# Performance work log

Measured on AMD Instinct MI355X. Metric: run time of the kernel, lower is better.

The kernel has to match this reference:

```python
import jax, jax.numpy as jnp
import numpy as np

B, I, O, T, L, K, PAD = 16, 256, 256, 512, 8192, 7, 3
EPS = 1e-8


def setup_inputs() -> dict:
    key = jax.random.key(0)
    ks = jax.random.split(key, 7)
    bx = jax.random.normal(ks[0], (B, I, L), dtype=jnp.float32)
    t = jax.random.normal(ks[1], (B, T), dtype=jnp.float32)
    # depthwise conv weight: torch Conv1d(groups=I) weight is (I, 1, K)
    conv_w = jax.random.normal(ks[2], (I, 1, K), dtype=jnp.float32) * (1.0 / np.sqrt(K))
    # 1x1 proj: torch Conv1d weight (O, I, 1) -> store as (O, I)
    proj_w = jax.random.normal(ks[3], (O, I), dtype=jnp.float32) * (1.0 / np.sqrt(I))
    proj_b = jax.random.normal(ks[4], (O,), dtype=jnp.float32) * 0.01
    # Linear(t_dim -> in_dim)
    mod_w = jax.random.normal(ks[5], (I, T), dtype=jnp.float32) * (1.0 / np.sqrt(T))
    mod_b = jax.random.normal(ks[6], (I,), dtype=jnp.float32) * 0.01
    return {"bx": bx, "t": t, "conv_w": conv_w, "proj_w": proj_w,
            "proj_b": proj_b, "mod_w": mod_w, "mod_b": mod_b}


def reference(bx, t, conv_w, proj_w, proj_b, mod_w, mod_b):
    # modulation: (B, I)
    mod = t @ mod_w.T + mod_b
    # per-sample modulated 1x1 weights: (B, O, I)
    bw = proj_w[None, :, :] * (mod[:, None, :] + 1.0)
    # demodulation (L2 over input dim, kernel dim is size 1)
    demod = jax.lax.rsqrt(jnp.sum(bw * bw, axis=2) + EPS)  # (B, O)
    bw = bw * demod[:, :, None]
    # depthwise conv over length, 'same' padding (kernel 7, pad 3)
    xc = jax.lax.conv_general_dilated(
        bx, conv_w,
        window_strides=(1,), padding=[(PAD, PAD)],
        dimension_numbers=('NCH', 'OIH', 'NCH'),
        feature_group_count=I)  # (B, I, L)
    # per-sample grouped 1x1 conv == batched matmul
    out = jnp.einsum('boi,bil->bol', bw, xc) + proj_b[None, :, None]
    return out
```

## Files before the change

kernel.cpp:

```cpp
#include <hip/hip_runtime.h>
#include <hip/hip_bf16.h>

#define B_ 16
#define I_ 256
#define O_ 256
#define T_ 512
#define L_ 8192
#define K_ 7
#define PAD_ 3
#define BN 64
#define LDK 264

typedef unsigned short u16;
typedef unsigned int u32;
typedef __attribute__((ext_vector_type(8))) short short8;
typedef __attribute__((ext_vector_type(4))) float f32x4;

__device__ inline u16 f2bf(float f) {
    union { float f; u32 u; } v; v.f = f;
    u32 r = v.u + 0x7FFF + ((v.u >> 16) & 1);
    return (u16)(r >> 16);
}

__global__ void mod_kernel(const float* __restrict__ t, const float* __restrict__ mod_w,
                           const float* __restrict__ mod_b, float* __restrict__ mod) {
    int g = blockIdx.x, b = blockIdx.y;
    int lane = threadIdx.x & 63, wv = threadIdx.x >> 6;
    const float* tb = t + b * T_;
    #pragma unroll
    for (int q = 0; q < 4; ++q) {
        int i = g * 16 + wv * 4 + q;
        const float* wr = mod_w + (size_t)i * T_;
        float s = 0.f;
        #pragma unroll
        for (int u = 0; u < 8; ++u) s += wr[lane + u * 64] * tb[lane + u * 64];
        #pragma unroll
        for (int d = 32; d; d >>= 1) s += __shfl_down(s, d);
        if (lane == 0) mod[b * I_ + i] = s + mod_b[i];
    }
}

__global__ void wmod_kernel(const float* __restrict__ proj_w, const float* __restrict__ mod,
                            u16* __restrict__ Wb) {
    int og = blockIdx.x, b = blockIdx.y;
    int lane = threadIdx.x & 63, wv = threadIdx.x >> 6;
    const float* mrow = mod + b * I_;
    #pragma unroll
    for (int q = 0; q < 4; ++q) {
        int o = og * 16 + wv * 4 + q;
        const float* pw = proj_w + (size_t)o * I_;
        float4 pv = *(const float4*)(pw + lane * 4);
        float4 mv = *(const float4*)(mrow + lane * 4);
        float v0 = pv.x * (mv.x + 1.f);
        float v1 = pv.y * (mv.y + 1.f);
        float v2 = pv.z * (mv.z + 1.f);
        float v3 = pv.w * (mv.w + 1.f);
        float ss = v0*v0 + v1*v1 + v2*v2 + v3*v3;
        #pragma unroll
        for (int d = 32; d; d >>= 1) ss += __shfl_xor(ss, d);
        float dem = rsqrtf(ss + 1e-8f);
        u32 lo = (u32)f2bf(v0 * dem) | ((u32)f2bf(v1 * dem) << 16);
        u32 hi = (u32)f2bf(v2 * dem) | ((u32)f2bf(v3 * dem) << 16);
        *(uint2*)(Wb + (size_t)(b * O_ + o) * I_ + lane * 4) = make_uint2(lo, hi);
    }
}

__global__ __launch_bounds__(256) void main_kernel(
    const float* __restrict__ bx, const float* __restrict__ conv_w,
    const u16* __restrict__ Wb, const float* __restrict__ proj_b,
    float* __restrict__ out)
{
    __shared__ __align__(16) u16 Xs[BN * LDK];

    const int tile = blockIdx.x;
    const int b = blockIdx.y;
    const int l0 = tile * BN;
    const int tid = threadIdx.x;
    const int lane = tid & 63;
    const int wv = tid >> 6;
    const int mlane = lane & 15;
    const int quad = lane >> 4;

    const int rq = tid >> 2;
    const int lq = tid & 3;
    const int i0 = rq * 4;
    const float* bxr = bx + (size_t)b * I_ * L_;
    const bool interior = (l0 >= 4) && (l0 + 72 <= L_);

    float wr[4][K_];
    #pragma unroll
    for (int di = 0; di < 4; ++di)
        #pragma unroll
        for (int j = 0; j < K_; ++j)
            wr[di][j] = conv_w[(i0 + di) * K_ + j];

    for (int it = 0; it < 4; ++it) {
        const int lb = it * 16 + lq * 4;
        u16 hv[4][4];
        #pragma unroll
        for (int di = 0; di < 4; ++di) {
            const float* row = bxr + (size_t)(i0 + di) * L_ + l0;
            float x[12];
            if (interior) {
                const float4* rp = (const float4*)(row + lb - 4);
                float4 w0 = rp[0], w1 = rp[1], w2 = rp[2];
                x[0]=w0.x; x[1]=w0.y; x[2]=w0.z; x[3]=w0.w;
                x[4]=w1.x; x[5]=w1.y; x[6]=w1.z; x[7]=w1.w;
                x[8]=w2.x; x[9]=w2.y; x[10]=w2.z; x[11]=w2.w;
            } else {
                #pragma unroll
                for (int w = 0; w < 12; ++w) {
                    int p = l0 + lb - 4 + w;
                    x[w] = (p >= 0 && p < L_) ? row[lb - 4 + w] : 0.f;
                }
            }
            #pragma unroll
            for (int dl = 0; dl < 4; ++dl) {
                float a = 0.f;
                #pragma unroll
                for (int j = 0; j < K_; ++j) a += wr[di][j] * x[dl + 1 + j];
                hv[dl][di] = f2bf(a);
            }
        }
        #pragma unroll
        for (int dl = 0; dl < 4; ++dl) {
            int n = lb + dl;
            u32 lo = (u32)hv[dl][0] | ((u32)hv[dl][1] << 16);
            u32 hi = (u32)hv[dl][2] | ((u32)hv[dl][3] << 16);
            *(uint2*)(&Xs[n * LDK + i0]) = make_uint2(lo, hi);
        }
    }
    __syncthreads();

    f32x4 acc[4][4];
    #pragma unroll
    for (int r = 0; r < 4; ++r)
        #pragma unroll
        for (int c = 0; c < 4; ++c)
            acc[r][c] = (f32x4){0.f, 0.f, 0.f, 0.f};

    const u16* Wrow = Wb + (size_t)(b * O_ + wv * 64 + mlane) * I_;

    for (int kb = 0; kb < 8; ++kb) {
        const int koff = kb * 32 + quad * 8;
        short8 a[4], bbf[4];
        #pragma unroll
        for (int r = 0; r < 4; ++r)
            a[r] = *(const short8*)(Wrow + r * 16 * I_ + koff);
        #pragma unroll
        for (int c = 0; c < 4; ++c)
            bbf[c] = *(const short8*)(&Xs[(c * 16 + mlane) * LDK + koff]);
        #pragma unroll
        for (int r = 0; r < 4; ++r)
            #pragma unroll
            for (int c = 0; c < 4; ++c)
                acc[r][c] = __builtin_amdgcn_mfma_f32_16x16x32_bf16(a[r], bbf[c], acc[r][c], 0, 0, 0);
    }

    float* outb = out + (size_t)b * O_ * L_;
    #pragma unroll
    for (int r = 0; r < 4; ++r) {
        const int obase = wv * 64 + r * 16 + quad * 4;
        #pragma unroll
        for (int p = 0; p < 4; ++p) {
            const int o = obase + p;
            const float bias = proj_b[o];
            float* orow = outb + (size_t)o * L_ + l0 + mlane;
            #pragma unroll
            for (int c = 0; c < 4; ++c)
                orow[c * 16] = acc[r][c][p] + bias;
        }
    }
}

extern "C" void kernel_launch(void* const* d_in, const int* in_sizes, int n_in,
                              void* d_out, int out_size, void* d_ws, size_t ws_size,
                              hipStream_t stream) {
    const float* bx     = (const float*)d_in[0];
    const float* t      = (const float*)d_in[1];
    const float* conv_w = (const float*)d_in[2];
    const float* proj_w = (const float*)d_in[3];
    const float* proj_b = (const float*)d_in[4];
    const float* mod_w  = (const float*)d_in[5];
    const float* mod_b  = (const float*)d_in[6];
    float* out = (float*)d_out;

    float* mod = (float*)d_ws;
    u16*   Wb  = (u16*)((char*)d_ws + 16384);

    mod_kernel<<<dim3(16, 16), 256, 0, stream>>>(t, mod_w, mod_b, mod);
    wmod_kernel<<<dim3(16, 16), 256, 0, stream>>>(proj_w, mod, Wb);
    main_kernel<<<dim3(128, 16), 256, 0, stream>>>(bx, conv_w, Wb, proj_b, out);
}
```

Measured before the change: 316.4 us.

## Split fused conv+GEMM kernel into separate conv and GEMM kernels via workspace

Splits the fused depthwise-conv plus MFMA GEMM kernel into two kernels when the workspace is large enough. The conv kernel writes a bf16 transposed tile to global memory, and the GEMM kernel reads it back directly without LDS. The aim is to decouple the conv phase's register and LDS pressure from the GEMM phase so that occupancy and latency hiding improve in each. In exchange it adds about 64 MB of extra global write and read traffic plus one more launch. The fused kernel remains as a fallback.

```diff
diff --git a/kernel.cpp b/kernel.cpp
--- a/kernel.cpp
+++ b/kernel.cpp
@@ -9,6 +9,7 @@
 #define K_ 7
 #define PAD_ 3
 #define BN 64
+#define NTILE 128
 #define LDK 264
 
 typedef unsigned short u16;
@@ -65,10 +66,8 @@
     }
 }
 
-__global__ __launch_bounds__(256) void main_kernel(
-    const float* __restrict__ bx, const float* __restrict__ conv_w,
-    const u16* __restrict__ Wb, const float* __restrict__ proj_b,
-    float* __restrict__ out)
+__global__ __launch_bounds__(256) void conv_kernel(
+    const float* __restrict__ bx, const float* __restrict__ conv_w, u16* __restrict__ xt)
 {
     __shared__ __align__(16) u16 Xs[BN * LDK];
 
@@ -76,10 +75,6 @@
     const int b = blockIdx.y;
     const int l0 = tile * BN;
     const int tid = threadIdx.x;
-    const int lane = tid & 63;
-    const int wv = tid >> 6;
-    const int mlane = lane & 15;
-    const int quad = lane >> 4;
 
     const int rq = tid >> 2;
     const int lq = tid & 3;
@@ -94,6 +89,7 @@
         for (int j = 0; j < K_; ++j)
             wr[di][j] = conv_w[(i0 + di) * K_ + j];
 
+    #pragma unroll
     for (int it = 0; it < 4; ++it) {
         const int lb = it * 16 + lq * 4;
         u16 hv[4][4];
@@ -132,6 +128,138 @@
     }
     __syncthreads();
 
+    u16* dst = xt + (size_t)(b * NTILE + tile) * (BN * I_);
+    #pragma unroll
+    for (int r = 0; r < 8; ++r) {
+        int g = tid + r * 256;
+        int n = g >> 5;
+        int c = g & 31;
+        uint4 v = *(const uint4*)(&Xs[n * LDK + c * 8]);
+        *(uint4*)(dst + (size_t)g * 8) = v;
+    }
+}
+
+__global__ __launch_bounds__(256) void gemm_kernel(
+    const u16* __restrict__ xt, const u16* __restrict__ Wb,
+    const float* __restrict__ proj_b, float* __restrict__ out)
+{
+    const int tile = blockIdx.x;
+    const int b = blockIdx.y;
+    const int l0 = tile * BN;
+    const int lane = threadIdx.x & 63;
+    const int wv = threadIdx.x >> 6;
+    const int mlane = lane & 15;
+    const int quad = lane >> 4;
+
+    f32x4 acc[4][4];
+    #pragma unroll
+    for (int r = 0; r < 4; ++r)
+        #pragma unroll
+        for (int c = 0; c < 4; ++c)
+            acc[r][c] = (f32x4){0.f, 0.f, 0.f, 0.f};
+
+    const u16* Wrow  = Wb + (size_t)(b * O_ + wv * 64 + mlane) * I_;
+    const u16* Xtile = xt + (size_t)(b * NTILE + tile) * (BN * I_);
+
+    for (int kb = 0; kb < 8; ++kb) {
+        const int koff = kb * 32 + quad * 8;
+        short8 a[4], bbf[4];
+        #pragma unroll
+        for (int r = 0; r < 4; ++r)
+            a[r] = *(const short8*)(Wrow + r * 16 * I_ + koff);
+        #pragma unroll
+        for (int c = 0; c < 4; ++c)
+            bbf[c] = *(const short8*)(Xtile + (c * 16 + mlane) * I_ + koff);
+        #pragma unroll
+        for (int r = 0; r < 4; ++r)
+            #pragma unroll
+            for (int c = 0; c < 4; ++c)
+                acc[r][c] = __builtin_amdgcn_mfma_f32_16x16x32_bf16(a[r], bbf[c], acc[r][c], 0, 0, 0);
+    }
+
+    float* outb = out + (size_t)b * O_ * L_;
+    #pragma unroll
+    for (int r = 0; r < 4; ++r) {
+        const int obase = wv * 64 + r * 16 + quad * 4;
+        #pragma unroll
+        for (int p = 0; p < 4; ++p) {
+            const int o = obase + p;
+            const float bias = proj_b[o];
+            float* orow = outb + (size_t)o * L_ + l0 + mlane;
+            #pragma unroll
+            for (int c = 0; c < 4; ++c)
+                orow[c * 16] = acc[r][c][p] + bias;
+        }
+    }
+}
+
+__global__ __launch_bounds__(256) void main_kernel(
+    const float* __restrict__ bx, const float* __restrict__ conv_w,
+    const u16* __restrict__ Wb, const float* __restrict__ proj_b,
+    float* __restrict__ out)
+{
+    __shared__ __align__(16) u16 Xs[BN * LDK];
+
+    const int tile = blockIdx.x;
+    const int b = blockIdx.y;
+    const int l0 = tile * BN;
+    const int tid = threadIdx.x;
+    const int lane = tid & 63;
+    const int wv = tid >> 6;
+    const int mlane = lane & 15;
+    const int quad = lane >> 4;
+
+    const int rq = tid >> 2;
+    const int lq = tid & 3;
+    const int i0 = rq * 4;
+    const float* bxr = bx + (size_t)b * I_ * L_;
+    const bool interior = (l0 >= 4) && (l0 + 72 <= L_);
+
+    float wr[4][K_];
+    #pragma unroll
+    for (int di = 0; di < 4; ++di)
+        #pragma unroll
+        for (int j = 0; j < K_; ++j)
+            wr[di][j] = conv_w[(i0 + di) * K_ + j];
+
+    for (int it = 0; it < 4; ++it) {
+        const int lb = it * 16 + lq * 4;
+        u16 hv[4][4];
+        #pragma unroll
+        for (int di = 0; di < 4; ++di) {
+            const float* row = bxr + (size_t)(i0 + di) * L_ + l0;
+            float x[12];
+            if (interior) {
+                const float4* rp = (const float4*)(row + lb - 4);
+                float4 w0 = rp[0], w1 = rp[1], w2 = rp[2];
+                x[0]=w0.x; x[1]=w0.y; x[2]=w0.z; x[3]=w0.w;
+                x[4]=w1.x; x[5]=w1.y; x[6]=w1.z; x[7]=w1.w;
+                x[8]=w2.x; x[9]=w2.y; x[10]=w2.z; x[11]=w2.w;
+            } else {
+                #pragma unroll
+                for (int w = 0; w < 12; ++w) {
+                    int p = l0 + lb - 4 + w;
+                    x[w] = (p >= 0 && p < L_) ? row[lb - 4 + w] : 0.f;
+                }
+            }
+            #pragma unroll
+            for (int dl = 0; dl < 4; ++dl) {
+                float a = 0.f;
+                #pragma unroll
+                for (int j = 0; j < K_; ++j) a += wr[di][j] * x[dl + 1 + j];
+                hv[dl][di] = f2bf(a);
+            }
+        }
+        #pragma unroll
+        for (int dl = 0; dl < 4; ++dl) {
+            int n = lb + dl;
+            u32 lo = (u32)hv[dl][0] | ((u32)hv[dl][1] << 16);
+            u32 hi = (u32)hv[dl][2] | ((u32)hv[dl][3] << 16);
+            *(uint2*)(&Xs[n * LDK + i0]) = make_uint2(lo, hi);
+        }
+    }
+    __syncthreads();
+
     f32x4 acc[4][4];
     #pragma unroll
     for (int r = 0; r < 4; ++r)
@@ -185,10 +313,20 @@
     const float* mod_b  = (const float*)d_in[6];
     float* out = (float*)d_out;
 
+    const size_t OFF_WB = 16384;
+    const size_t OFF_XT = OFF_WB + (size_t)B_ * O_ * I_ * 2ull;
+    const size_t need   = OFF_XT + (size_t)B_ * NTILE * BN * I_ * 2ull;
+
     float* mod = (float*)d_ws;
-    u16*   Wb  = (u16*)((char*)d_ws + 16384);
+    u16*   Wb  = (u16*)((char*)d_ws + OFF_WB);
+    u16*   xt  = (u16*)((char*)d_ws + OFF_XT);
 
     mod_kernel<<<dim3(16, 16), 256, 0, stream>>>(t, mod_w, mod_b, mod);
     wmod_kernel<<<dim3(16, 16), 256, 0, stream>>>(proj_w, mod, Wb);
-    main_kernel<<<dim3(128, 16), 256, 0, stream>>>(bx, conv_w, Wb, proj_b, out);
-}
+    if (ws_size >= need) {
+        conv_kernel<<<dim3(NTILE, 16), 256, 0, stream>>>(bx, conv_w, xt);
+        gemm_kernel<<<dim3(NTILE, 16), 256, 0, stream>>>(xt, Wb, proj_b, out);
+    } else {
+        main_kernel<<<dim3(NTILE, 16), 256, 0, stream>>>(bx, conv_w, Wb, proj_b, out);
+    }
+}
```

Measured after the change: 366.3 us. +15.8%, slower.

## Split conv and GEMM into separate kernels with MFMA-swizzled global layouts

Applied to the files above, without the earlier changes.

Merges the modulation and demodulation kernels into one per-batch kernel that writes weights pre-swizzled in MFMA fragment order. The depthwise conv moves to its own kernel, which writes bf16 activations to global workspace in the same fragment-native layout. A new GEMM kernel loads fragments directly with coalesced 16-byte loads, double-buffers the k-loop in registers, and stages output through LDS so stores are float4 and row-contiguous. This removes the strided output stores and the per-tile LDS transpose, but adds a global round trip of the bf16 activations (about 64MB written and read).

```diff
diff --git a/kernel.cpp b/kernel.cpp
--- a/kernel.cpp
+++ b/kernel.cpp
@@ -7,9 +7,8 @@
 #define T_ 512
 #define L_ 8192
 #define K_ 7
-#define PAD_ 3
-#define BN 64
-#define LDK 264
+#define CT 1024
+#define NT 128
 
 typedef unsigned short u16;
 typedef unsigned int u32;
@@ -22,115 +21,121 @@
     return (u16)(r >> 16);
 }
 
-__global__ void mod_kernel(const float* __restrict__ t, const float* __restrict__ mod_w,
-                           const float* __restrict__ mod_b, float* __restrict__ mod) {
-    int g = blockIdx.x, b = blockIdx.y;
-    int lane = threadIdx.x & 63, wv = threadIdx.x >> 6;
+
+__global__ __launch_bounds__(256) void wmod_kernel(
+    const float* __restrict__ t, const float* __restrict__ mod_w, const float* __restrict__ mod_b,
+    const float* __restrict__ proj_w, u16* __restrict__ Wsw)
+{
+    __shared__ __align__(16) float mod_s[I_];
+    const int b = blockIdx.x, tid = threadIdx.x;
+
     const float* tb = t + b * T_;
-    #pragma unroll
-    for (int q = 0; q < 4; ++q) {
-        int i = g * 16 + wv * 4 + q;
-        const float* wr = mod_w + (size_t)i * T_;
-        float s = 0.f;
-        #pragma unroll
-        for (int u = 0; u < 8; ++u) s += wr[lane + u * 64] * tb[lane + u * 64];
-        #pragma unroll
-        for (int d = 32; d; d >>= 1) s += __shfl_down(s, d);
-        if (lane == 0) mod[b * I_ + i] = s + mod_b[i];
-    }
-}
-
-__global__ void wmod_kernel(const float* __restrict__ proj_w, const float* __restrict__ mod,
-                            u16* __restrict__ Wb) {
-    int og = blockIdx.x, b = blockIdx.y;
-    int lane = threadIdx.x & 63, wv = threadIdx.x >> 6;
-    const float* mrow = mod + b * I_;
-    #pragma unroll
-    for (int q = 0; q < 4; ++q) {
-        int o = og * 16 + wv * 4 + q;
-        const float* pw = proj_w + (size_t)o * I_;
-        float4 pv = *(const float4*)(pw + lane * 4);
-        float4 mv = *(const float4*)(mrow + lane * 4);
-        float v0 = pv.x * (mv.x + 1.f);
-        float v1 = pv.y * (mv.y + 1.f);
-        float v2 = pv.z * (mv.z + 1.f);
-        float v3 = pv.w * (mv.w + 1.f);
-        float ss = v0*v0 + v1*v1 + v2*v2 + v3*v3;
-        #pragma unroll
-        for (int d = 32; d; d >>= 1) ss += __shfl_xor(ss, d);
-        float dem = rsqrtf(ss + 1e-8f);
-        u32 lo = (u32)f2bf(v0 * dem) | ((u32)f2bf(v1 * dem) << 16);
-        u32 hi = (u32)f2bf(v2 * dem) | ((u32)f2bf(v3 * dem) << 16);
-        *(uint2*)(Wb + (size_t)(b * O_ + o) * I_ + lane * 4) = make_uint2(lo, hi);
-    }
-}
-
-__global__ __launch_bounds__(256) void main_kernel(
-    const float* __restrict__ bx, const float* __restrict__ conv_w,
-    const u16* __restrict__ Wb, const float* __restrict__ proj_b,
-    float* __restrict__ out)
+    const float* wr = mod_w + (size_t)tid * T_;
+    float s = 0.f;
+    #pragma unroll 8
+    for (int k = 0; k < T_ / 4; ++k) {
+        float4 w4 = *(const float4*)(wr + 4 * k);
+        float4 t4 = *(const float4*)(tb + 4 * k);
+        s += w4.x * t4.x + w4.y * t4.y + w4.z * t4.z + w4.w * t4.w;
+    }
+    mod_s[tid] = s + mod_b[tid];
+    __syncthreads();
+
+    const float* pw = proj_w + (size_t)tid * I_;
+    float ss = 0.f;
+    #pragma unroll 8
+    for (int k = 0; k < I_ / 4; ++k) {
+        float4 p = *(const float4*)(pw + 4 * k);
+        float4 m = *(const float4*)(&mod_s[4 * k]);
+        float a0 = p.x * (m.x + 1.f), a1 = p.y * (m.y + 1.f);
+        float a2 = p.z * (m.z + 1.f), a3 = p.w * (m.w + 1.f);
+        ss += a0 * a0 + a1 * a1 + a2 * a2 + a3 * a3;
+    }
+    const float dem = rsqrtf(ss + 1e-8f);
+    const int wv = tid >> 6, r = (tid >> 4) & 3, ml = tid & 15;
+    #pragma unroll 4
+    for (int oc = 0; oc < 32; ++oc) {
+        float4 p0 = *(const float4*)(pw + oc * 8);
+        float4 p1 = *(const float4*)(pw + oc * 8 + 4);
+        float4 m0 = *(const float4*)(&mod_s[oc * 8]);
+        float4 m1 = *(const float4*)(&mod_s[oc * 8 + 4]);
+        u32 q0 = (u32)f2bf(p0.x * (m0.x + 1.f) * dem) | ((u32)f2bf(p0.y * (m0.y + 1.f) * dem) << 16);
+        u32 q1 = (u32)f2bf(p0.z * (m0.z + 1.f) * dem) | ((u32)f2bf(p0.w * (m0.w + 1.f) * dem) << 16);
+        u32 q2 = (u32)f2bf(p1.x * (m1.x + 1.f) * dem) | ((u32)f2bf(p1.y * (m1.y + 1.f) * dem) << 16);
+        u32 q3 = (u32)f2bf(p1.z * (m1.z + 1.f) * dem) | ((u32)f2bf(p1.w * (m1.w + 1.f) * dem) << 16);
+        const int kb = oc >> 2, quad = oc & 3;
+        u16* dst = Wsw + ((((size_t)(b * 4 + wv) * 8 + kb) * 4 + r) * 64 + quad * 16 + ml) * 8;
+        *(uint4*)dst = make_uint4(q0, q1, q2, q3);
+    }
+}
+
+__global__ __launch_bounds__(256) void conv_kernel(
+    const float* __restrict__ bx, const float* __restrict__ conv_w, u16* __restrict__ Xsw)
 {
-    __shared__ __align__(16) u16 Xs[BN * LDK];
-
-    const int tile = blockIdx.x;
-    const int b = blockIdx.y;
-    const int l0 = tile * BN;
+    __shared__ __align__(16) u16 Os[CT * 8];
+    const int oct = blockIdx.x;
+    const int lg  = blockIdx.y;
+    const int b   = blockIdx.z;
     const int tid = threadIdx.x;
-    const int lane = tid & 63;
-    const int wv = tid >> 6;
-    const int mlane = lane & 15;
-    const int quad = lane >> 4;
-
-    const int rq = tid >> 2;
-    const int lq = tid & 3;
-    const int i0 = rq * 4;
-    const float* bxr = bx + (size_t)b * I_ * L_;
-    const bool interior = (l0 >= 4) && (l0 + 72 <= L_);
-
-    float wr[4][K_];
-    #pragma unroll
-    for (int di = 0; di < 4; ++di)
+    const int l0  = lg * CT;
+    const int lt  = l0 + tid * 4;
+    const float* base = bx + ((size_t)b * I_ + oct * 8) * L_;
+
+    float w[8][K_];
+    #pragma unroll
+    for (int ch = 0; ch < 8; ++ch)
         #pragma unroll
         for (int j = 0; j < K_; ++j)
-            wr[di][j] = conv_w[(i0 + di) * K_ + j];
-
-    for (int it = 0; it < 4; ++it) {
-        const int lb = it * 16 + lq * 4;
-        u16 hv[4][4];
-        #pragma unroll
-        for (int di = 0; di < 4; ++di) {
-            const float* row = bxr + (size_t)(i0 + di) * L_ + l0;
-            float x[12];
-            if (interior) {
-                const float4* rp = (const float4*)(row + lb - 4);
-                float4 w0 = rp[0], w1 = rp[1], w2 = rp[2];
-                x[0]=w0.x; x[1]=w0.y; x[2]=w0.z; x[3]=w0.w;
-                x[4]=w1.x; x[5]=w1.y; x[6]=w1.z; x[7]=w1.w;
-                x[8]=w2.x; x[9]=w2.y; x[10]=w2.z; x[11]=w2.w;
-            } else {
-                #pragma unroll
-                for (int w = 0; w < 12; ++w) {
-                    int p = l0 + lb - 4 + w;
-                    x[w] = (p >= 0 && p < L_) ? row[lb - 4 + w] : 0.f;
-                }
-            }
-            #pragma unroll
-            for (int dl = 0; dl < 4; ++dl) {
-                float a = 0.f;
-                #pragma unroll
-                for (int j = 0; j < K_; ++j) a += wr[di][j] * x[dl + 1 + j];
-                hv[dl][di] = f2bf(a);
-            }
+            w[ch][j] = conv_w[(oct * 8 + ch) * K_ + j];
+
+    const bool okL = (lt > 0);
+    const bool okR = (lt + 4 < L_);
+    u32 pk[4][4] = {};
+
+    #pragma unroll
+    for (int ch = 0; ch < 8; ++ch) {
+        const float* row = base + (size_t)ch * L_;
+        float4 za = okL ? *(const float4*)(row + lt - 4) : make_float4(0.f, 0.f, 0.f, 0.f);
+        float4 zb = *(const float4*)(row + lt);
+        float4 zc = okR ? *(const float4*)(row + lt + 4) : make_float4(0.f, 0.f, 0.f, 0.f);
+        float x[12] = {za.x, za.y, za.z, za.w, zb.x, zb.y, zb.z, zb.w, zc.x, zc.y, zc.z, zc.w};
+        #pragma unroll
+        for (int dl = 0; dl < 4; ++dl) {
+            float a = 0.f;
+            #pragma unroll
+            for (int j = 0; j < K_; ++j) a += w[ch][j] * x[dl + 1 + j];
+            pk[dl][ch >> 1] |= ((u32)f2bf(a)) << (16 * (ch & 1));
         }
-        #pragma unroll
-        for (int dl = 0; dl < 4; ++dl) {
-            int n = lb + dl;
-            u32 lo = (u32)hv[dl][0] | ((u32)hv[dl][1] << 16);
-            u32 hi = (u32)hv[dl][2] | ((u32)hv[dl][3] << 16);
-            *(uint2*)(&Xs[n * LDK + i0]) = make_uint2(lo, hi);
-        }
-    }
+    }
+    #pragma unroll
+    for (int dl = 0; dl < 4; ++dl)
+        *(uint4*)(&Os[(size_t)(tid * 4 + dl) * 8]) = make_uint4(pk[dl][0], pk[dl][1], pk[dl][2], pk[dl][3]);
     __syncthreads();
+
+    const int kb = oct >> 2, quad = oct & 3;
+    #pragma unroll
+    for (int pass = 0; pass < 4; ++pass) {
+        int idx = pass * 256 + tid;
+        int l = l0 + idx;
+        int tile = l >> 6, c = (l >> 4) & 3, ml = l & 15;
+        uint4 v = *(const uint4*)(&Os[(size_t)idx * 8]);
+        u16* dst = Xsw + ((((size_t)(b * NT + tile) * 8 + kb) * 4 + c) * 64 + quad * 16 + ml) * 8;
+        *(uint4*)dst = v;
+    }
+}
+
+__global__ __launch_bounds__(256) void gemm_kernel(
+    const u16* __restrict__ Xsw, const u16* __restrict__ Wsw,
+    const float* __restrict__ proj_b, float* __restrict__ out)
+{
+    __shared__ __align__(16) float Cs[64 * 68];
+    const int tile = blockIdx.x, b = blockIdx.y;
+    const int tid = threadIdx.x, lane = tid & 63, wv = tid >> 6;
+    const int ml = lane & 15, quad = lane >> 4;
+    const int l0 = tile * 64;
+
+    const u16* Ab = Wsw + ((size_t)(b * 4 + wv) * 8 * 4 * 64) * 8 + (size_t)lane * 8;
+    const u16* Bb = Xsw + ((size_t)(b * NT + tile) * 8 * 4 * 64) * 8 + (size_t)lane * 8;
 
     f32x4 acc[4][4];
     #pragma unroll
@@ -139,37 +144,47 @@
         for (int c = 0; c < 4; ++c)
             acc[r][c] = (f32x4){0.f, 0.f, 0.f, 0.f};
 
-    const u16* Wrow = Wb + (size_t)(b * O_ + wv * 64 + mlane) * I_;
-
+    short8 a[2][4], bb[2][4];
+    #pragma unroll
+    for (int r = 0; r < 4; ++r) a[0][r] = *(const short8*)(Ab + (size_t)r * 512);
+    #pragma unroll
+    for (int c = 0; c < 4; ++c) bb[0][c] = *(const short8*)(Bb + (size_t)c * 512);
+
+    #pragma unroll
     for (int kb = 0; kb < 8; ++kb) {
-        const int koff = kb * 32 + quad * 8;
-        short8 a[4], bbf[4];
+        const int cur = kb & 1, nxt = cur ^ 1;
+        if (kb < 7) {
+            #pragma unroll
+            for (int r = 0; r < 4; ++r) a[nxt][r] = *(const short8*)(Ab + (size_t)((kb + 1) * 4 + r) * 512);
+            #pragma unroll
+            for (int c = 0; c < 4; ++c) bb[nxt][c] = *(const short8*)(Bb + (size_t)((kb + 1) * 4 + c) * 512);
+        }
         #pragma unroll
         for (int r = 0; r < 4; ++r)
-            a[r] = *(const short8*)(Wrow + r * 16 * I_ + koff);
+            #pragma unroll
+            for (int c = 0; c < 4; ++c)
+                acc[r][c] = __builtin_amdgcn_mfma_f32_16x16x32_bf16(a[cur][r], bb[cur][c], acc[r][c], 0, 0, 0);
+    }
+
+    #pragma unroll
+    for (int r = 0; r < 4; ++r) {
+        float4 pb = *(const float4*)(proj_b + wv * 64 + r * 16 + quad * 4);
+        float pbv[4] = {pb.x, pb.y, pb.z, pb.w};
         #pragma unroll
         for (int c = 0; c < 4; ++c)
-            bbf[c] = *(const short8*)(&Xs[(c * 16 + mlane) * LDK + koff]);
-        #pragma unroll
-        for (int r = 0; r < 4; ++r)
-            #pragma unroll
-            for (int c = 0; c < 4; ++c)
-                acc[r][c] = __builtin_amdgcn_mfma_f32_16x16x32_bf16(a[r], bbf[c], acc[r][c], 0, 0, 0);
-    }
-
-    float* outb = out + (size_t)b * O_ * L_;
-    #pragma unroll
-    for (int r = 0; r < 4; ++r) {
-        const int obase = wv * 64 + r * 16 + quad * 4;
-        #pragma unroll
-        for (int p = 0; p < 4; ++p) {
-            const int o = obase + p;
-            const float bias = proj_b[o];
-            float* orow = outb + (size_t)o * L_ + l0 + mlane;
-            #pragma unroll
-            for (int c = 0; c < 4; ++c)
-                orow[c * 16] = acc[r][c][p] + bias;
+            #pragma unroll
+            for (int p = 0; p < 4; ++p)
+                Cs[(wv * 16 + quad * 4 + p) * 68 + c * 16 + ml] = acc[r][c][p] + pbv[p];
+        __syncthreads();
+        #pragma unroll
+        for (int q = 0; q < 4; ++q) {
+            int g = q * 256 + tid;
+            int orow = g >> 4, lq = g & 15;
+            float4 v = *(const float4*)(&Cs[orow * 68 + lq * 4]);
+            int o = (orow >> 4) * 64 + r * 16 + (orow & 15);
+            *(float4*)(out + ((size_t)b * O_ + o) * L_ + l0 + lq * 4) = v;
         }
+        __syncthreads();
     }
 }
 
@@ -185,10 +200,10 @@
     const float* mod_b  = (const float*)d_in[6];
     float* out = (float*)d_out;
 
-    float* mod = (float*)d_ws;
-    u16*   Wb  = (u16*)((char*)d_ws + 16384);
-
-    mod_kernel<<<dim3(16, 16), 256, 0, stream>>>(t, mod_w, mod_b, mod);
-    wmod_kernel<<<dim3(16, 16), 256, 0, stream>>>(proj_w, mod, Wb);
-    main_kernel<<<dim3(128, 16), 256, 0, stream>>>(bx, conv_w, Wb, proj_b, out);
-}
+    u16* Wsw = (u16*)d_ws;
+    u16* Xsw = (u16*)((char*)d_ws + (size_t)B_ * 4 * 8 * 4 * 64 * 8 * 2);
+
+    wmod_kernel<<<dim3(B_), 256, 0, stream>>>(t, mod_w, mod_b, proj_w, Wsw);
+    conv_kernel<<<dim3(32, L_ / CT, B_), 256, 0, stream>>>(bx, conv_w, Xsw);
+    gemm_kernel<<<dim3(NT, B_), 256, 0, stream>>>(Xsw, Wsw, proj_b, out);
+}
```

After: 316.4 us. About the same (+0.0%).
